# Kernel optimization log

Measured on AMD Instinct MI355X. Metric: run time of the kernel, lower is better.

## Reference

```python
import jax, jax.numpy as jnp
import numpy as np

N = 100000   # nodes
E = 1600000  # edges
F = 128      # input node features
H = 128      # hidden channels
G = 512      # graphs in batch
EPS = 1e-5   # BatchNorm eps


def setup_inputs() -> dict:
    key = jax.random.key(0)
    ks = jax.random.split(key, 24)
    x = jax.random.normal(ks[0], (N, F), jnp.float32)
    edge_index = jax.random.randint(ks[1], (2, E), 0, N)
    batch = jnp.sort(jax.random.randint(ks[2], (N,), 0, G))

    def lin_w(k, i, o):
        return jax.random.normal(k, (i, o), jnp.float32) / np.sqrt(i)

    inp = {
        "x": x, "edge_index": edge_index, "batch": batch,
        "W1": lin_w(ks[3], F, H), "b1": jnp.zeros((H,), jnp.float32),
        "g1": jnp.ones((H,), jnp.float32), "be1": jnp.zeros((H,), jnp.float32),
        "m1": 0.1 * jax.random.normal(ks[4], (H,), jnp.float32),
        "v1": jax.random.uniform(ks[5], (H,), jnp.float32) + 0.5,
        "W2": lin_w(ks[6], H, H), "b2": jnp.zeros((H,), jnp.float32),
        "g2": jnp.ones((H,), jnp.float32), "be2": jnp.zeros((H,), jnp.float32),
        "m2": 0.1 * jax.random.normal(ks[7], (H,), jnp.float32),
        "v2": jax.random.uniform(ks[8], (H,), jnp.float32) + 0.5,
        "W3": lin_w(ks[9], H, H), "b3": jnp.zeros((H,), jnp.float32),
        "g3": jnp.ones((H,), jnp.float32), "be3": jnp.zeros((H,), jnp.float32),
        "m3": 0.1 * jax.random.normal(ks[10], (H,), jnp.float32),
        "v3": jax.random.uniform(ks[11], (H,), jnp.float32) + 0.5,
        "Wl": lin_w(ks[12], H, 1), "bl": jnp.zeros((1,), jnp.float32),
    }
    return inp


def _gcn_norm(edge_index):
    # add self-loops, then symmetric normalization deg^-1/2 A_hat deg^-1/2
    loops = jnp.arange(N)
    src = jnp.concatenate([edge_index[0], loops])
    dst = jnp.concatenate([edge_index[1], loops])
    deg = jax.ops.segment_sum(jnp.ones_like(src, jnp.float32), dst, num_segments=N)
    dinv = jax.lax.rsqrt(jnp.maximum(deg, 1.0))
    norm = dinv[src] * dinv[dst]  # [E+N]
    return src, dst, norm


def _gcn_conv(x, W, b, src, dst, norm):
    h = x @ W                                    # [N,H] dense GEMM first (PyG order)
    msg = h[src] * norm[:, None]                 # gather + scale, [E+N,H]
    agg = jax.ops.segment_sum(msg, dst, num_segments=N)  # scatter-add
    return agg + b


def _bn_relu(x, g, be, m, v):
    # inference BatchNorm1d (running stats) + ReLU
    return jax.nn.relu((x - m) * jax.lax.rsqrt(v + EPS) * g + be)


def reference(x, edge_index, batch,
              W1, b1, g1, be1, m1, v1,
              W2, b2, g2, be2, m2, v2,
              W3, b3, g3, be3, m3, v3,
              Wl, bl):
    src, dst, norm = _gcn_norm(edge_index)
    h = _bn_relu(_gcn_conv(x, W1, b1, src, dst, norm), g1, be1, m1, v1)
    h = _bn_relu(_gcn_conv(h, W2, b2, src, dst, norm), g2, be2, m2, v2)
    h = _bn_relu(_gcn_conv(h, W3, b3, src, dst, norm), g3, be3, m3, v3)
    # global mean pool over graphs
    sums = jax.ops.segment_sum(h, batch, num_segments=G)           # [G,H]
    cnt = jax.ops.segment_sum(jnp.ones((N,), jnp.float32), batch, num_segments=G)
    pooled = sums / jnp.maximum(cnt, 1.0)[:, None]
    # dropout is identity at inference; final linear
    return pooled @ Wl + bl  # [G,1]
```

## Files before the change

### kernel.cpp

```cpp
#include <hip/hip_runtime.h>
#include <hip/hip_bf16.h>

#define NN 100000
#define NE 1600000
#define HD 128
#define NG 512
#define BN_EPS 1e-5f

#define GEMM_BLOCKS 1563

#define BIN_SHIFT 8
#define NBIN 391
#define TILE 16384
#define NBLK_BIN 98

typedef __attribute__((ext_vector_type(8))) short short8;
typedef __attribute__((ext_vector_type(4))) float floatx4;

__device__ __forceinline__ ushort f2bf(float f) {
    union { float f; uint u; } v; v.f = f;
    uint r = (v.u + 0x7FFF + ((v.u >> 16) & 1)) >> 16;
    return (ushort)r;
}
__device__ __forceinline__ float bflo(uint u) { union { uint u; float f; } v; v.u = u << 16; return v.f; }
__device__ __forceinline__ float bfhi(uint u) { union { uint u; float f; } v; v.u = u & 0xFFFF0000u; return v.f; }

__global__ void k_prep_all(const float* __restrict__ W1, const float* __restrict__ W2,
                           const float* __restrict__ W3,
                           ushort* __restrict__ Wt1, ushort* __restrict__ Wt2,
                           ushort* __restrict__ Wt3,
                           const float* __restrict__ b1, const float* __restrict__ g1,
                           const float* __restrict__ be1, const float* __restrict__ m1,
                           const float* __restrict__ v1,
                           const float* __restrict__ b2, const float* __restrict__ g2,
                           const float* __restrict__ be2, const float* __restrict__ m2,
                           const float* __restrict__ v2,
                           const float* __restrict__ b3, const float* __restrict__ g3,
                           const float* __restrict__ be3, const float* __restrict__ m3,
                           const float* __restrict__ v3,
                           float* scale1, float* shift1, float* scale2, float* shift2,
                           float* scale3, float* shift3,
                           const int* __restrict__ bat, float* __restrict__ invcnt,
                           float* __restrict__ out2d) {
    int blk = blockIdx.x, tid = threadIdx.x;
    if (blk < 192) {
        int w = blk >> 6;
        int i = (blk & 63) * 256 + tid;
        const float* W = (w == 0) ? W1 : (w == 1) ? W2 : W3;
        ushort* Wt = (w == 0) ? Wt1 : (w == 1) ? Wt2 : Wt3;
        int k = i >> 7, n = i & 127;
        Wt[n * 128 + k] = f2bf(W[i]);
    } else if (blk < 195) {
        if (tid < 128) {
            int l = blk - 192;
            const float *b, *g, *be, *m, *v;
            float *sc, *sh;
            if (l == 0)      { b = b1; g = g1; be = be1; m = m1; v = v1; sc = scale1; sh = shift1; }
            else if (l == 1) { b = b2; g = g2; be = be2; m = m2; v = v2; sc = scale2; sh = shift2; }
            else             { b = b3; g = g3; be = be3; m = m3; v = v3; sc = scale3; sh = shift3; }
            float s = g[tid] * rsqrtf(v[tid] + BN_EPS);
            sc[tid] = s;
            sh[tid] = (b[tid] - m[tid]) * s + be[tid];
        }
    } else {
        int g = (blk - 195) * 256 + tid;
        if (g < NG) {
            int lo = 0, hi = NN;
            while (lo < hi) { int mid = (lo + hi) >> 1; if (bat[mid] < g) lo = mid + 1; else hi = mid; }
            int lo2 = lo, hi2 = NN;
            while (lo2 < hi2) { int mid = (lo2 + hi2) >> 1; if (bat[mid] < g + 1) lo2 = mid + 1; else hi2 = mid; }
            int cnt = lo2 - lo;
            invcnt[g] = 1.f / fmaxf((float)cnt, 1.f);
#pragma unroll
            for (int i = 0; i < 8; ++i) out2d[g * 8 + i] = 0.f;
        }
    }
}

__launch_bounds__(256)
__global__ void k_fused1(const float* __restrict__ x, const ushort* __restrict__ Wt,
                         ushort* __restrict__ hs,
                         const int* __restrict__ dst, int* __restrict__ L) {
    __shared__ int lh[NBIN];
    const int tid = threadIdx.x;
    if (blockIdx.x >= GEMM_BLOCKS) {
        int blk = blockIdx.x - GEMM_BLOCKS;
        for (int i = tid; i < NBIN; i += 256) lh[i] = 0;
        __syncthreads();
        long base = (long)blk * TILE;
#pragma unroll 4
        for (int i = 0; i < TILE / 256; ++i) {
            long e = base + i * 256 + tid;
            if (e < NE) atomicAdd(&lh[dst[e] >> BIN_SHIFT], 1);
        }
        __syncthreads();
        for (int i = tid; i < NBIN; i += 256) L[i * NBLK_BIN + blk] = lh[i];
        return;
    }
    const int wave = tid >> 6, lane = tid & 63;
    const int m = lane & 15, kg = lane >> 4;
    const long row0 = (long)blockIdx.x * 64 + wave * 16;

    long arow = row0 + m;
    long arc = arow < NN ? arow : (NN - 1);
    const float* xf = x + arc * 128;
    short8 a[4];
#pragma unroll
    for (int s = 0; s < 4; ++s) {
        float4 f0 = *(const float4*)(xf + s * 32 + kg * 8);
        float4 f1 = *(const float4*)(xf + s * 32 + kg * 8 + 4);
        short8 t;
        t[0] = (short)f2bf(f0.x); t[1] = (short)f2bf(f0.y);
        t[2] = (short)f2bf(f0.z); t[3] = (short)f2bf(f0.w);
        t[4] = (short)f2bf(f1.x); t[5] = (short)f2bf(f1.y);
        t[6] = (short)f2bf(f1.z); t[7] = (short)f2bf(f1.w);
        a[s] = t;
    }

    floatx4 acc[8];
#pragma unroll
    for (int ct = 0; ct < 8; ++ct) acc[ct] = (floatx4){0.f, 0.f, 0.f, 0.f};

#pragma unroll
    for (int s = 0; s < 4; ++s) {
#pragma unroll
        for (int ct = 0; ct < 8; ++ct) {
            short8 b = *(const short8*)(Wt + (ct * 16 + m) * 128 + s * 32 + kg * 8);
            acc[ct] = __builtin_amdgcn_mfma_f32_16x16x32_bf16(a[s], b, acc[ct], 0, 0, 0);
        }
    }

#pragma unroll
    for (int r = 0; r < 4; ++r) {
        long orow = row0 + kg * 4 + r;
        if (orow < NN) {
#pragma unroll
            for (int ct = 0; ct < 8; ++ct)
                hs[orow * 128 + ct * 16 + m] = f2bf(acc[ct][r]);
        }
    }
}

__global__ void k_binscan(int* __restrict__ L, int* __restrict__ bin_ebase,
                          int* __restrict__ rs) {
    __shared__ int s[512];
    int t = threadIdx.x;
    int tot = 0;
    if (t < NBIN) {
        int run = 0;
        for (int b = 0; b < NBLK_BIN; ++b) {
            int h = L[t * NBLK_BIN + b];
            L[t * NBLK_BIN + b] = run;
            run += h;
        }
        tot = run;
    }
    s[t] = tot;
    __syncthreads();
    for (int o = 1; o < 512; o <<= 1) {
        int x = (t >= o) ? s[t - o] : 0;
        __syncthreads();
        s[t] += x;
        __syncthreads();
    }
    int excl = s[t] - tot;
    if (t < NBIN) {
        bin_ebase[t] = excl;
        for (int b = 0; b < NBLK_BIN; ++b) L[t * NBLK_BIN + b] += excl;
    }
    if (t == 0) { bin_ebase[NBIN] = NE; rs[NN] = NE; }
}

__launch_bounds__(256)
__global__ void k_binscatter(const int* __restrict__ src, const int* __restrict__ dst,
                             const int* __restrict__ L, uint* __restrict__ bpack) {
    __shared__ int off[NBIN];
    int t = threadIdx.x, blk = blockIdx.x;
    for (int i = t; i < NBIN; i += 256) off[i] = L[i * NBLK_BIN + blk];
    __syncthreads();
    long base = (long)blk * TILE;
#pragma unroll 4
    for (int i = 0; i < TILE / 256; ++i) {
        long e = base + i * 256 + t;
        if (e < NE) {
            int d = dst[e];
            int p = atomicAdd(&off[d >> BIN_SHIFT], 1);
            bpack[p] = (uint)src[e] | ((uint)(d & 255) << 24);
        }
    }
}

__launch_bounds__(256)
__global__ void k_bincsr(const uint* __restrict__ bpack, const int* __restrict__ bin_ebase,
                         int* __restrict__ rs, float* __restrict__ dinv,
                         int* __restrict__ csr) {
    __shared__ int cnt[256];
    __shared__ int sc[256];
    __shared__ int run[256];
    int t = threadIdx.x, b = blockIdx.x;
    int e0 = bin_ebase[b], e1 = bin_ebase[b + 1];
    cnt[t] = 0;
    __syncthreads();
    for (int e = e0 + t; e < e1; e += 256) atomicAdd(&cnt[bpack[e] >> 24], 1);
    __syncthreads();
    int c = cnt[t];
    sc[t] = c;
    __syncthreads();
    for (int o = 1; o < 256; o <<= 1) {
        int x = (t >= o) ? sc[t - o] : 0;
        __syncthreads();
        sc[t] += x;
        __syncthreads();
    }
    int excl = sc[t] - c;
    int node = (b << BIN_SHIFT) + t;
    if (node < NN) {
        rs[node] = e0 + excl;
        dinv[node] = rsqrtf((float)(c + 1));
    }
    run[t] = e0 + excl;
    __syncthreads();
    for (int e = e0 + t; e < e1; e += 256) {
        uint u = bpack[e];
        int p = atomicAdd(&run[u >> 24], 1);
        csr[p] = (int)(u & 0xFFFFFFu);
    }
}

#define WT_STRIDE 136
__launch_bounds__(256)
__global__ void k_gemm_l23(const ushort* __restrict__ xb, const ushort* __restrict__ Wt,
                           const float* __restrict__ dinv, ushort* __restrict__ hs) {
    __shared__ ushort sWt[128 * WT_STRIDE];
    const int tid = threadIdx.x;
    for (int i = tid; i < 2048; i += 256) {
        int row = i >> 4, seg = i & 15;
        *(uint4*)&sWt[row * WT_STRIDE + seg * 8] = *(const uint4*)(Wt + row * 128 + seg * 8);
    }
    __syncthreads();

    const int wave = tid >> 6, lane = tid & 63;
    const int m = lane & 15, kg = lane >> 4;
    const long row0 = (long)blockIdx.x * 64 + wave * 16;

    long arow = row0 + m;
    long arc = arow < NN ? arow : (NN - 1);
    short8 a[4];
#pragma unroll
    for (int s = 0; s < 4; ++s)
        a[s] = *(const short8*)(xb + arc * 128 + s * 32 + kg * 8);

    floatx4 acc[8];
#pragma unroll
    for (int ct = 0; ct < 8; ++ct) acc[ct] = (floatx4){0.f, 0.f, 0.f, 0.f};

#pragma unroll
    for (int s = 0; s < 4; ++s) {
#pragma unroll
        for (int ct = 0; ct < 8; ++ct) {
            short8 b = *(const short8*)&sWt[(ct * 16 + m) * WT_STRIDE + s * 32 + kg * 8];
            acc[ct] = __builtin_amdgcn_mfma_f32_16x16x32_bf16(a[s], b, acc[ct], 0, 0, 0);
        }
    }

#pragma unroll
    for (int r = 0; r < 4; ++r) {
        long orow = row0 + kg * 4 + r;
        if (orow < NN) {
            float dd = dinv[orow];
#pragma unroll
            for (int ct = 0; ct < 8; ++ct)
                hs[orow * 128 + ct * 16 + m] = f2bf(acc[ct][r] * dd);
        }
    }
}

template <bool SCALE_SRC, bool POOL>
__launch_bounds__(256)
__global__ void k_gather_w(const ushort* __restrict__ hs, const int* __restrict__ rs,
                           const int* __restrict__ csr, const float* __restrict__ dinv,
                           const float* __restrict__ scale, const float* __restrict__ shift,
                           ushort* __restrict__ xout,
                           const int* __restrict__ bat, const float* __restrict__ invcnt,
                           const float* __restrict__ Wl, float* __restrict__ out2d) {
    const int tid = threadIdx.x;
    const int d = blockIdx.x * 4 + (tid >> 6);
    const int lane = tid & 63;
    const int sub = lane >> 4;
    const int c0 = (lane & 15) * 8;

    const int e0 = rs[d], e1 = rs[d + 1];
    const float dd = dinv[d];

    float a0 = 0.f, a1 = 0.f, a2 = 0.f, a3 = 0.f,
          a4 = 0.f, a5 = 0.f, a6 = 0.f, a7 = 0.f;

    if (sub == 0) {
        uint4 sv = *(const uint4*)(hs + (long)d * 128 + c0);
        float w = SCALE_SRC ? dd : 1.0f;
        a0 = w * bflo(sv.x); a1 = w * bfhi(sv.x);
        a2 = w * bflo(sv.y); a3 = w * bfhi(sv.y);
        a4 = w * bflo(sv.z); a5 = w * bfhi(sv.z);
        a6 = w * bflo(sv.w); a7 = w * bfhi(sv.w);
    }

    int j = e0 + sub;
    int s0 = 0, s1 = 0, s2 = 0, s3 = 0;
    bool have = (j + 12 < e1);
    if (have) { s0 = csr[j]; s1 = csr[j + 4]; s2 = csr[j + 8]; s3 = csr[j + 12]; }
    while (have) {
        int jn = j + 16;
        bool nxt = (jn + 12 < e1);
        int n0 = 0, n1 = 0, n2 = 0, n3 = 0;
        if (nxt) { n0 = csr[jn]; n1 = csr[jn + 4]; n2 = csr[jn + 8]; n3 = csr[jn + 12]; }
        float w0 = 1.f, w1 = 1.f, w2 = 1.f, w3 = 1.f;
        if (SCALE_SRC) { w0 = dinv[s0]; w1 = dinv[s1]; w2 = dinv[s2]; w3 = dinv[s3]; }
        uint4 v0 = *(const uint4*)(hs + (long)s0 * 128 + c0);
        uint4 v1 = *(const uint4*)(hs + (long)s1 * 128 + c0);
        uint4 v2 = *(const uint4*)(hs + (long)s2 * 128 + c0);
        uint4 v3 = *(const uint4*)(hs + (long)s3 * 128 + c0);
        a0 += w0 * bflo(v0.x) + w1 * bflo(v1.x) + w2 * bflo(v2.x) + w3 * bflo(v3.x);
        a1 += w0 * bfhi(v0.x) + w1 * bfhi(v1.x) + w2 * bfhi(v2.x) + w3 * bfhi(v3.x);
        a2 += w0 * bflo(v0.y) + w1 * bflo(v1.y) + w2 * bflo(v2.y) + w3 * bflo(v3.y);
        a3 += w0 * bfhi(v0.y) + w1 * bfhi(v1.y) + w2 * bfhi(v2.y) + w3 * bfhi(v3.y);
        a4 += w0 * bflo(v0.z) + w1 * bflo(v1.z) + w2 * bflo(v2.z) + w3 * bflo(v3.z);
        a5 += w0 * bfhi(v0.z) + w1 * bfhi(v1.z) + w2 * bfhi(v2.z) + w3 * bfhi(v3.z);
        a6 += w0 * bflo(v0.w) + w1 * bflo(v1.w) + w2 * bflo(v2.w) + w3 * bflo(v3.w);
        a7 += w0 * bfhi(v0.w) + w1 * bfhi(v1.w) + w2 * bfhi(v2.w) + w3 * bfhi(v3.w);
        j = jn; s0 = n0; s1 = n1; s2 = n2; s3 = n3; have = nxt;
    }
    if (j < e1) {
        bool b1 = (j + 4) < e1, b2 = (j + 8) < e1;
        int t0 = csr[j];
        int t1 = b1 ? csr[j + 4] : t0;
        int t2 = b2 ? csr[j + 8] : t0;
        float w0 = SCALE_SRC ? dinv[t0] : 1.f;
        float w1 = b1 ? (SCALE_SRC ? dinv[t1] : 1.f) : 0.f;
        float w2 = b2 ? (SCALE_SRC ? dinv[t2] : 1.f) : 0.f;
        uint4 v0 = *(const uint4*)(hs + (long)t0 * 128 + c0);
        uint4 v1 = *(const uint4*)(hs + (long)t1 * 128 + c0);
        uint4 v2 = *(const uint4*)(hs + (long)t2 * 128 + c0);
        a0 += w0 * bflo(v0.x) + w1 * bflo(v1.x) + w2 * bflo(v2.x);
        a1 += w0 * bfhi(v0.x) + w1 * bfhi(v1.x) + w2 * bfhi(v2.x);
        a2 += w0 * bflo(v0.y) + w1 * bflo(v1.y) + w2 * bflo(v2.y);
        a3 += w0 * bfhi(v0.y) + w1 * bfhi(v1.y) + w2 * bfhi(v2.y);
        a4 += w0 * bflo(v0.z) + w1 * bflo(v1.z) + w2 * bflo(v2.z);
        a5 += w0 * bfhi(v0.z) + w1 * bfhi(v1.z) + w2 * bfhi(v2.z);
        a6 += w0 * bflo(v0.w) + w1 * bflo(v1.w) + w2 * bflo(v2.w);
        a7 += w0 * bfhi(v0.w) + w1 * bfhi(v1.w) + w2 * bfhi(v2.w);
    }

    a0 += __shfl_xor(a0, 16); a1 += __shfl_xor(a1, 16);
    a2 += __shfl_xor(a2, 16); a3 += __shfl_xor(a3, 16);
    a4 += __shfl_xor(a4, 16); a5 += __shfl_xor(a5, 16);
    a6 += __shfl_xor(a6, 16); a7 += __shfl_xor(a7, 16);
    a0 += __shfl_xor(a0, 32); a1 += __shfl_xor(a1, 32);
    a2 += __shfl_xor(a2, 32); a3 += __shfl_xor(a3, 32);
    a4 += __shfl_xor(a4, 32); a5 += __shfl_xor(a5, 32);
    a6 += __shfl_xor(a6, 32); a7 += __shfl_xor(a7, 32);

    float pd = 0.f;
    if (sub == 0) {
        float4 sca = *(const float4*)(scale + c0);
        float4 scb = *(const float4*)(scale + c0 + 4);
        float4 sha = *(const float4*)(shift + c0);
        float4 shb = *(const float4*)(shift + c0 + 4);
        float r0 = fmaxf(dd * a0 * sca.x + sha.x, 0.f);
        float r1 = fmaxf(dd * a1 * sca.y + sha.y, 0.f);
        float r2 = fmaxf(dd * a2 * sca.z + sha.z, 0.f);
        float r3 = fmaxf(dd * a3 * sca.w + sha.w, 0.f);
        float r4 = fmaxf(dd * a4 * scb.x + shb.x, 0.f);
        float r5 = fmaxf(dd * a5 * scb.y + shb.y, 0.f);
        float r6 = fmaxf(dd * a6 * scb.z + shb.z, 0.f);
        float r7 = fmaxf(dd * a7 * scb.w + shb.w, 0.f);
        if constexpr (POOL) {
            float4 wa = *(const float4*)(Wl + c0);
            float4 wb = *(const float4*)(Wl + c0 + 4);
            pd = r0 * wa.x + r1 * wa.y + r2 * wa.z + r3 * wa.w +
                 r4 * wb.x + r5 * wb.y + r6 * wb.z + r7 * wb.w;
        } else {
            uint4 o;
            o.x = (uint)f2bf(r0) | ((uint)f2bf(r1) << 16);
            o.y = (uint)f2bf(r2) | ((uint)f2bf(r3) << 16);
            o.z = (uint)f2bf(r4) | ((uint)f2bf(r5) << 16);
            o.w = (uint)f2bf(r6) | ((uint)f2bf(r7) << 16);
            *(uint4*)(xout + (long)d * 128 + c0) = o;
        }
    }
    if constexpr (POOL) {
        pd += __shfl_xor(pd, 1);
        pd += __shfl_xor(pd, 2);
        pd += __shfl_xor(pd, 4);
        pd += __shfl_xor(pd, 8);
        if (lane == 0) {
            int g = bat[d];
            atomicAdd(&out2d[g * 8 + (d & 7)], pd * invcnt[g]);
        }
    }
}

__global__ void k_final(const float* __restrict__ out2d, const float* __restrict__ bl,
                        float* __restrict__ out) {
    int g = blockIdx.x * 256 + threadIdx.x;
    if (g >= NG) return;
    float s = bl[0];
#pragma unroll
    for (int i = 0; i < 8; ++i) s += out2d[g * 8 + i];
    out[g] = s;
}

extern "C" void kernel_launch(void* const* d_in, const int* in_sizes, int n_in,
                              void* d_out, int out_size, void* d_ws, size_t ws_size,
                              hipStream_t stream) {
    const float* x   = (const float*)d_in[0];
    const int*   ei  = (const int*)d_in[1];
    const int*   bat = (const int*)d_in[2];
    const float* W1  = (const float*)d_in[3];
    const float* b1  = (const float*)d_in[4];
    const float* g1  = (const float*)d_in[5];
    const float* be1 = (const float*)d_in[6];
    const float* m1  = (const float*)d_in[7];
    const float* v1  = (const float*)d_in[8];
    const float* W2  = (const float*)d_in[9];
    const float* b2  = (const float*)d_in[10];
    const float* g2  = (const float*)d_in[11];
    const float* be2 = (const float*)d_in[12];
    const float* m2  = (const float*)d_in[13];
    const float* v2  = (const float*)d_in[14];
    const float* W3  = (const float*)d_in[15];
    const float* b3  = (const float*)d_in[16];
    const float* g3  = (const float*)d_in[17];
    const float* be3 = (const float*)d_in[18];
    const float* m3  = (const float*)d_in[19];
    const float* v3  = (const float*)d_in[20];
    const float* Wl  = (const float*)d_in[21];
    const float* bl  = (const float*)d_in[22];
    float* out = (float*)d_out;

    const int* srcp = ei;
    const int* dstp = ei + NE;

    char* ws = (char*)d_ws;
    size_t off = 0;
    auto alloc = [&](size_t bytes) { char* p = ws + off; off += (bytes + 255) & ~255ULL; return p; };
    float*  dinv     = (float*) alloc(NN * 4);
    int*    rs       = (int*)   alloc((NN + 1) * 4);
    int*    L        = (int*)   alloc((size_t)NBIN * NBLK_BIN * 4);
    int*    bin_ebase= (int*)   alloc((NBIN + 1) * 4);
    uint*   bpack    = (uint*)  alloc((size_t)NE * 4);
    int*    csr      = (int*)   alloc((size_t)NE * 4);
    float*  scale1 = (float*) alloc(HD * 4);
    float*  shift1 = (float*) alloc(HD * 4);
    float*  scale2 = (float*) alloc(HD * 4);
    float*  shift2 = (float*) alloc(HD * 4);
    float*  scale3 = (float*) alloc(HD * 4);
    float*  shift3 = (float*) alloc(HD * 4);
    float*  invcnt = (float*) alloc(NG * 4);
    float*  out2d  = (float*) alloc(NG * 8 * 4);
    ushort* Wt1    = (ushort*)alloc(128 * 128 * 2);
    ushort* Wt2    = (ushort*)alloc(128 * 128 * 2);
    ushort* Wt3    = (ushort*)alloc(128 * 128 * 2);
    ushort* hs     = (ushort*)alloc((size_t)NN * HD * 2);
    ushort* xbuf   = (ushort*)alloc((size_t)NN * HD * 2);

    const int gath_grid = NN / 4;

    k_prep_all<<<197, 256, 0, stream>>>(W1, W2, W3, Wt1, Wt2, Wt3,
                                        b1, g1, be1, m1, v1, b2, g2, be2, m2, v2,
                                        b3, g3, be3, m3, v3,
                                        scale1, shift1, scale2, shift2, scale3, shift3,
                                        bat, invcnt, out2d);

    k_fused1<<<GEMM_BLOCKS + NBLK_BIN, 256, 0, stream>>>(x, Wt1, hs, dstp, L);

    k_binscan<<<1, 512, 0, stream>>>(L, bin_ebase, rs);
    k_binscatter<<<NBLK_BIN, 256, 0, stream>>>(srcp, dstp, L, bpack);
    k_bincsr<<<NBIN, 256, 0, stream>>>(bpack, bin_ebase, rs, dinv, csr);

    k_gather_w<true, false><<<gath_grid, 256, 0, stream>>>(
        hs, rs, csr, dinv, scale1, shift1, xbuf, nullptr, nullptr, nullptr, nullptr);
    k_gemm_l23<<<GEMM_BLOCKS, 256, 0, stream>>>(xbuf, Wt2, dinv, hs);
    k_gather_w<false, false><<<gath_grid, 256, 0, stream>>>(
        hs, rs, csr, dinv, scale2, shift2, xbuf, nullptr, nullptr, nullptr, nullptr);
    k_gemm_l23<<<GEMM_BLOCKS, 256, 0, stream>>>(xbuf, Wt3, dinv, hs);
    k_gather_w<false, true><<<gath_grid, 256, 0, stream>>>(
        hs, rs, csr, dinv, scale3, shift3, nullptr, bat, invcnt, Wl, out2d);

    k_final<<<2, 256, 0, stream>>>(out2d, bl, out);
}
```

Baseline: 513.5 us.

## Parallelize bin scan across blocks, shrink binning tiles, use persistent gather grid

The edge-binning count/scatter now uses 391 smaller tiles instead of 98 large ones, giving more parallel blocks. The single-block serial bin scan is replaced by a two-stage scan: one block per bin scans per-tile counts, and a second kernel scans the bin totals. The bin base offset is then added inside the scatter. The three gather kernels switch from one wave per node to a fixed 2048-block grid-stride loop, which cuts block launch overhead but may worsen load balance across nodes of uneven degree.

```diff
diff --git a/kernel.cpp b/kernel.cpp
--- a/kernel.cpp
+++ b/kernel.cpp
@@ -8,11 +8,12 @@
 #define BN_EPS 1e-5f
 
 #define GEMM_BLOCKS 1563
+#define GATH_BLOCKS 2048
 
 #define BIN_SHIFT 8
 #define NBIN 391
-#define TILE 16384
-#define NBLK_BIN 98
+#define TILE 4096
+#define NBLK_BIN 391
 
 typedef __attribute__((ext_vector_type(8))) short short8;
 typedef __attribute__((ext_vector_type(4))) float floatx4;
@@ -141,21 +142,28 @@
     }
 }
 
-__global__ void k_binscan(int* __restrict__ L, int* __restrict__ bin_ebase,
-                          int* __restrict__ rs) {
+__global__ void k_scanA(int* __restrict__ L, int* __restrict__ binTot) {
+    __shared__ int s[512];
+    int b = blockIdx.x, t = threadIdx.x;
+    int v = (t < NBLK_BIN) ? L[b * NBLK_BIN + t] : 0;
+    s[t] = v;
+    __syncthreads();
+    for (int o = 1; o < 512; o <<= 1) {
+        int x = (t >= o) ? s[t - o] : 0;
+        __syncthreads();
+        s[t] += x;
+        __syncthreads();
+    }
+    if (t < NBLK_BIN) L[b * NBLK_BIN + t] = s[t] - v;
+    if (t == 511) binTot[b] = s[511];
+}
+
+__global__ void k_scanB(const int* __restrict__ binTot, int* __restrict__ bin_ebase,
+                        int* __restrict__ rs) {
     __shared__ int s[512];
     int t = threadIdx.x;
-    int tot = 0;
-    if (t < NBIN) {
-        int run = 0;
-        for (int b = 0; b < NBLK_BIN; ++b) {
-            int h = L[t * NBLK_BIN + b];
-            L[t * NBLK_BIN + b] = run;
-            run += h;
-        }
-        tot = run;
-    }
-    s[t] = tot;
+    int v = (t < NBIN) ? binTot[t] : 0;
+    s[t] = v;
     __syncthreads();
     for (int o = 1; o < 512; o <<= 1) {
         int x = (t >= o) ? s[t - o] : 0;
@@ -163,20 +171,17 @@
         s[t] += x;
         __syncthreads();
     }
-    int excl = s[t] - tot;
-    if (t < NBIN) {
-        bin_ebase[t] = excl;
-        for (int b = 0; b < NBLK_BIN; ++b) L[t * NBLK_BIN + b] += excl;
-    }
+    if (t < NBIN) bin_ebase[t] = s[t] - v;
     if (t == 0) { bin_ebase[NBIN] = NE; rs[NN] = NE; }
 }
 
 __launch_bounds__(256)
 __global__ void k_binscatter(const int* __restrict__ src, const int* __restrict__ dst,
-                             const int* __restrict__ L, uint* __restrict__ bpack) {
+                             const int* __restrict__ L, const int* __restrict__ bin_ebase,
+                             uint* __restrict__ bpack) {
     __shared__ int off[NBIN];
     int t = threadIdx.x, blk = blockIdx.x;
-    for (int i = t; i < NBIN; i += 256) off[i] = L[i * NBLK_BIN + blk];
+    for (int i = t; i < NBIN; i += 256) off[i] = L[i * NBLK_BIN + blk] + bin_ebase[i];
     __syncthreads();
     long base = (long)blk * TILE;
 #pragma unroll 4
@@ -284,117 +289,120 @@
                            const int* __restrict__ bat, const float* __restrict__ invcnt,
                            const float* __restrict__ Wl, float* __restrict__ out2d) {
     const int tid = threadIdx.x;
-    const int d = blockIdx.x * 4 + (tid >> 6);
+    const int gw = blockIdx.x * 4 + (tid >> 6);
+    const int NW = GATH_BLOCKS * 4;
     const int lane = tid & 63;
     const int sub = lane >> 4;
     const int c0 = (lane & 15) * 8;
 
-    const int e0 = rs[d], e1 = rs[d + 1];
-    const float dd = dinv[d];
-
-    float a0 = 0.f, a1 = 0.f, a2 = 0.f, a3 = 0.f,
-          a4 = 0.f, a5 = 0.f, a6 = 0.f, a7 = 0.f;
-
-    if (sub == 0) {
-        uint4 sv = *(const uint4*)(hs + (long)d * 128 + c0);
-        float w = SCALE_SRC ? dd : 1.0f;
-        a0 = w * bflo(sv.x); a1 = w * bfhi(sv.x);
-        a2 = w * bflo(sv.y); a3 = w * bfhi(sv.y);
-        a4 = w * bflo(sv.z); a5 = w * bfhi(sv.z);
-        a6 = w * bflo(sv.w); a7 = w * bfhi(sv.w);
-    }
-
-    int j = e0 + sub;
-    int s0 = 0, s1 = 0, s2 = 0, s3 = 0;
-    bool have = (j + 12 < e1);
-    if (have) { s0 = csr[j]; s1 = csr[j + 4]; s2 = csr[j + 8]; s3 = csr[j + 12]; }
-    while (have) {
-        int jn = j + 16;
-        bool nxt = (jn + 12 < e1);
-        int n0 = 0, n1 = 0, n2 = 0, n3 = 0;
-        if (nxt) { n0 = csr[jn]; n1 = csr[jn + 4]; n2 = csr[jn + 8]; n3 = csr[jn + 12]; }
-        float w0 = 1.f, w1 = 1.f, w2 = 1.f, w3 = 1.f;
-        if (SCALE_SRC) { w0 = dinv[s0]; w1 = dinv[s1]; w2 = dinv[s2]; w3 = dinv[s3]; }
-        uint4 v0 = *(const uint4*)(hs + (long)s0 * 128 + c0);
-        uint4 v1 = *(const uint4*)(hs + (long)s1 * 128 + c0);
-        uint4 v2 = *(const uint4*)(hs + (long)s2 * 128 + c0);
-        uint4 v3 = *(const uint4*)(hs + (long)s3 * 128 + c0);
-        a0 += w0 * bflo(v0.x) + w1 * bflo(v1.x) + w2 * bflo(v2.x) + w3 * bflo(v3.x);
-        a1 += w0 * bfhi(v0.x) + w1 * bfhi(v1.x) + w2 * bfhi(v2.x) + w3 * bfhi(v3.x);
-        a2 += w0 * bflo(v0.y) + w1 * bflo(v1.y) + w2 * bflo(v2.y) + w3 * bflo(v3.y);
-        a3 += w0 * bfhi(v0.y) + w1 * bfhi(v1.y) + w2 * bfhi(v2.y) + w3 * bfhi(v3.y);
-        a4 += w0 * bflo(v0.z) + w1 * bflo(v1.z) + w2 * bflo(v2.z) + w3 * bflo(v3.z);
-        a5 += w0 * bfhi(v0.z) + w1 * bfhi(v1.z) + w2 * bfhi(v2.z) + w3 * bfhi(v3.z);
-        a6 += w0 * bflo(v0.w) + w1 * bflo(v1.w) + w2 * bflo(v2.w) + w3 * bflo(v3.w);
-        a7 += w0 * bfhi(v0.w) + w1 * bfhi(v1.w) + w2 * bfhi(v2.w) + w3 * bfhi(v3.w);
-        j = jn; s0 = n0; s1 = n1; s2 = n2; s3 = n3; have = nxt;
-    }
-    if (j < e1) {
-        bool b1 = (j + 4) < e1, b2 = (j + 8) < e1;
-        int t0 = csr[j];
-        int t1 = b1 ? csr[j + 4] : t0;
-        int t2 = b2 ? csr[j + 8] : t0;
-        float w0 = SCALE_SRC ? dinv[t0] : 1.f;
-        float w1 = b1 ? (SCALE_SRC ? dinv[t1] : 1.f) : 0.f;
-        float w2 = b2 ? (SCALE_SRC ? dinv[t2] : 1.f) : 0.f;
-        uint4 v0 = *(const uint4*)(hs + (long)t0 * 128 + c0);
-        uint4 v1 = *(const uint4*)(hs + (long)t1 * 128 + c0);
-        uint4 v2 = *(const uint4*)(hs + (long)t2 * 128 + c0);
-        a0 += w0 * bflo(v0.x) + w1 * bflo(v1.x) + w2 * bflo(v2.x);
-        a1 += w0 * bfhi(v0.x) + w1 * bfhi(v1.x) + w2 * bfhi(v2.x);
-        a2 += w0 * bflo(v0.y) + w1 * bflo(v1.y) + w2 * bflo(v2.y);
-        a3 += w0 * bfhi(v0.y) + w1 * bfhi(v1.y) + w2 * bfhi(v2.y);
-        a4 += w0 * bflo(v0.z) + w1 * bflo(v1.z) + w2 * bflo(v2.z);
-        a5 += w0 * bfhi(v0.z) + w1 * bfhi(v1.z) + w2 * bfhi(v2.z);
-        a6 += w0 * bflo(v0.w) + w1 * bflo(v1.w) + w2 * bflo(v2.w);
-        a7 += w0 * bfhi(v0.w) + w1 * bfhi(v1.w) + w2 * bfhi(v2.w);
-    }
-
-    a0 += __shfl_xor(a0, 16); a1 += __shfl_xor(a1, 16);
-    a2 += __shfl_xor(a2, 16); a3 += __shfl_xor(a3, 16);
-    a4 += __shfl_xor(a4, 16); a5 += __shfl_xor(a5, 16);
-    a6 += __shfl_xor(a6, 16); a7 += __shfl_xor(a7, 16);
-    a0 += __shfl_xor(a0, 32); a1 += __shfl_xor(a1, 32);
-    a2 += __shfl_xor(a2, 32); a3 += __shfl_xor(a3, 32);
-    a4 += __shfl_xor(a4, 32); a5 += __shfl_xor(a5, 32);
-    a6 += __shfl_xor(a6, 32); a7 += __shfl_xor(a7, 32);
-
-    float pd = 0.f;
-    if (sub == 0) {
-        float4 sca = *(const float4*)(scale + c0);
-        float4 scb = *(const float4*)(scale + c0 + 4);
-        float4 sha = *(const float4*)(shift + c0);
-        float4 shb = *(const float4*)(shift + c0 + 4);
-        float r0 = fmaxf(dd * a0 * sca.x + sha.x, 0.f);
-        float r1 = fmaxf(dd * a1 * sca.y + sha.y, 0.f);
-        float r2 = fmaxf(dd * a2 * sca.z + sha.z, 0.f);
-        float r3 = fmaxf(dd * a3 * sca.w + sha.w, 0.f);
-        float r4 = fmaxf(dd * a4 * scb.x + shb.x, 0.f);
-        float r5 = fmaxf(dd * a5 * scb.y + shb.y, 0.f);
-        float r6 = fmaxf(dd * a6 * scb.z + shb.z, 0.f);
-        float r7 = fmaxf(dd * a7 * scb.w + shb.w, 0.f);
+    for (int d = gw; d < NN; d += NW) {
+        const int e0 = rs[d], e1 = rs[d + 1];
+        const float dd = dinv[d];
+
+        float a0 = 0.f, a1 = 0.f, a2 = 0.f, a3 = 0.f,
+              a4 = 0.f, a5 = 0.f, a6 = 0.f, a7 = 0.f;
+
+        if (sub == 0) {
+            uint4 sv = *(const uint4*)(hs + (long)d * 128 + c0);
+            float w = SCALE_SRC ? dd : 1.0f;
+            a0 = w * bflo(sv.x); a1 = w * bfhi(sv.x);
+            a2 = w * bflo(sv.y); a3 = w * bfhi(sv.y);
+            a4 = w * bflo(sv.z); a5 = w * bfhi(sv.z);
+            a6 = w * bflo(sv.w); a7 = w * bfhi(sv.w);
+        }
+
+        int j = e0 + sub;
+        int s0 = 0, s1 = 0, s2 = 0, s3 = 0;
+        bool have = (j + 12 < e1);
+        if (have) { s0 = csr[j]; s1 = csr[j + 4]; s2 = csr[j + 8]; s3 = csr[j + 12]; }
+        while (have) {
+            int jn = j + 16;
+            bool nxt = (jn + 12 < e1);
+            int n0 = 0, n1 = 0, n2 = 0, n3 = 0;
+            if (nxt) { n0 = csr[jn]; n1 = csr[jn + 4]; n2 = csr[jn + 8]; n3 = csr[jn + 12]; }
+            float w0 = 1.f, w1 = 1.f, w2 = 1.f, w3 = 1.f;
+            if (SCALE_SRC) { w0 = dinv[s0]; w1 = dinv[s1]; w2 = dinv[s2]; w3 = dinv[s3]; }
+            uint4 v0 = *(const uint4*)(hs + (long)s0 * 128 + c0);
+            uint4 v1 = *(const uint4*)(hs + (long)s1 * 128 + c0);
+            uint4 v2 = *(const uint4*)(hs + (long)s2 * 128 + c0);
+            uint4 v3 = *(const uint4*)(hs + (long)s3 * 128 + c0);
+            a0 += w0 * bflo(v0.x) + w1 * bflo(v1.x) + w2 * bflo(v2.x) + w3 * bflo(v3.x);
+            a1 += w0 * bfhi(v0.x) + w1 * bfhi(v1.x) + w2 * bfhi(v2.x) + w3 * bfhi(v3.x);
+            a2 += w0 * bflo(v0.y) + w1 * bflo(v1.y) + w2 * bflo(v2.y) + w3 * bflo(v3.y);
+            a3 += w0 * bfhi(v0.y) + w1 * bfhi(v1.y) + w2 * bfhi(v2.y) + w3 * bfhi(v3.y);
+            a4 += w0 * bflo(v0.z) + w1 * bflo(v1.z) + w2 * bflo(v2.z) + w3 * bflo(v3.z);
+            a5 += w0 * bfhi(v0.z) + w1 * bfhi(v1.z) + w2 * bfhi(v2.z) + w3 * bfhi(v3.z);
+            a6 += w0 * bflo(v0.w) + w1 * bflo(v1.w) + w2 * bflo(v2.w) + w3 * bflo(v3.w);
+            a7 += w0 * bfhi(v0.w) + w1 * bfhi(v1.w) + w2 * bfhi(v2.w) + w3 * bfhi(v3.w);
+            j = jn; s0 = n0; s1 = n1; s2 = n2; s3 = n3; have = nxt;
+        }
+        if (j < e1) {
+            bool b1 = (j + 4) < e1, b2 = (j + 8) < e1;
+            int t0 = csr[j];
+            int t1 = b1 ? csr[j + 4] : t0;
+            int t2 = b2 ? csr[j + 8] : t0;
+            float w0 = SCALE_SRC ? dinv[t0] : 1.f;
+            float w1 = b1 ? (SCALE_SRC ? dinv[t1] : 1.f) : 0.f;
+            float w2 = b2 ? (SCALE_SRC ? dinv[t2] : 1.f) : 0.f;
+            uint4 v0 = *(const uint4*)(hs + (long)t0 * 128 + c0);
+            uint4 v1 = *(const uint4*)(hs + (long)t1 * 128 + c0);
+            uint4 v2 = *(const uint4*)(hs + (long)t2 * 128 + c0);
+            a0 += w0 * bflo(v0.x) + w1 * bflo(v1.x) + w2 * bflo(v2.x);
+            a1 += w0 * bfhi(v0.x) + w1 * bfhi(v1.x) + w2 * bfhi(v2.x);
+            a2 += w0 * bflo(v0.y) + w1 * bflo(v1.y) + w2 * bflo(v2.y);
+            a3 += w0 * bfhi(v0.y) + w1 * bfhi(v1.y) + w2 * bfhi(v2.y);
+            a4 += w0 * bflo(v0.z) + w1 * bflo(v1.z) + w2 * bflo(v2.z);
+            a5 += w0 * bfhi(v0.z) + w1 * bfhi(v1.z) + w2 * bfhi(v2.z);
+            a6 += w0 * bflo(v0.w) + w1 * bflo(v1.w) + w2 * bflo(v2.w);
+            a7 += w0 * bfhi(v0.w) + w1 * bfhi(v1.w) + w2 * bfhi(v2.w);
+        }
+
+        a0 += __shfl_xor(a0, 16); a1 += __shfl_xor(a1, 16);
+        a2 += __shfl_xor(a2, 16); a3 += __shfl_xor(a3, 16);
+        a4 += __shfl_xor(a4, 16); a5 += __shfl_xor(a5, 16);
+        a6 += __shfl_xor(a6, 16); a7 += __shfl_xor(a7, 16);
+        a0 += __shfl_xor(a0, 32); a1 += __shfl_xor(a1, 32);
+        a2 += __shfl_xor(a2, 32); a3 += __shfl_xor(a3, 32);
+        a4 += __shfl_xor(a4, 32); a5 += __shfl_xor(a5, 32);
+        a6 += __shfl_xor(a6, 32); a7 += __shfl_xor(a7, 32);
+
+        float pd = 0.f;
+        if (sub == 0) {
+            float4 sca = *(const float4*)(scale + c0);
+            float4 scb = *(const float4*)(scale + c0 + 4);
+            float4 sha = *(const float4*)(shift + c0);
+            float4 shb = *(const float4*)(shift + c0 + 4);
+            float r0 = fmaxf(dd * a0 * sca.x + sha.x, 0.f);
+            float r1 = fmaxf(dd * a1 * sca.y + sha.y, 0.f);
+            float r2 = fmaxf(dd * a2 * sca.z + sha.z, 0.f);
+            float r3 = fmaxf(dd * a3 * sca.w + sha.w, 0.f);
+            float r4 = fmaxf(dd * a4 * scb.x + shb.x, 0.f);
+            float r5 = fmaxf(dd * a5 * scb.y + shb.y, 0.f);
+            float r6 = fmaxf(dd * a6 * scb.z + shb.z, 0.f);
+            float r7 = fmaxf(dd * a7 * scb.w + shb.w, 0.f);
+            if constexpr (POOL) {
+                float4 wa = *(const float4*)(Wl + c0);
+                float4 wb = *(const float4*)(Wl + c0 + 4);
+                pd = r0 * wa.x + r1 * wa.y + r2 * wa.z + r3 * wa.w +
+                     r4 * wb.x + r5 * wb.y + r6 * wb.z + r7 * wb.w;
+            } else {
+                uint4 o;
+                o.x = (uint)f2bf(r0) | ((uint)f2bf(r1) << 16);
+                o.y = (uint)f2bf(r2) | ((uint)f2bf(r3) << 16);
+                o.z = (uint)f2bf(r4) | ((uint)f2bf(r5) << 16);
+                o.w = (uint)f2bf(r6) | ((uint)f2bf(r7) << 16);
+                *(uint4*)(xout + (long)d * 128 + c0) = o;
+            }
+        }
         if constexpr (POOL) {
-            float4 wa = *(const float4*)(Wl + c0);
-            float4 wb = *(const float4*)(Wl + c0 + 4);
-            pd = r0 * wa.x + r1 * wa.y + r2 * wa.z + r3 * wa.w +
-                 r4 * wb.x + r5 * wb.y + r6 * wb.z + r7 * wb.w;
-        } else {
-            uint4 o;
-            o.x = (uint)f2bf(r0) | ((uint)f2bf(r1) << 16);
-            o.y = (uint)f2bf(r2) | ((uint)f2bf(r3) << 16);
-            o.z = (uint)f2bf(r4) | ((uint)f2bf(r5) << 16);
-            o.w = (uint)f2bf(r6) | ((uint)f2bf(r7) << 16);
-            *(uint4*)(xout + (long)d * 128 + c0) = o;
-        }
-    }
-    if constexpr (POOL) {
-        pd += __shfl_xor(pd, 1);
-        pd += __shfl_xor(pd, 2);
-        pd += __shfl_xor(pd, 4);
-        pd += __shfl_xor(pd, 8);
-        if (lane == 0) {
-            int g = bat[d];
-            atomicAdd(&out2d[g * 8 + (d & 7)], pd * invcnt[g]);
+            pd += __shfl_xor(pd, 1);
+            pd += __shfl_xor(pd, 2);
+            pd += __shfl_xor(pd, 4);
+            pd += __shfl_xor(pd, 8);
+            if (lane == 0) {
+                int g = bat[d];
+                atomicAdd(&out2d[g * 8 + (d & 7)], pd * invcnt[g]);
+            }
         }
     }
 }
@@ -446,6 +454,7 @@
     float*  dinv     = (float*) alloc(NN * 4);
     int*    rs       = (int*)   alloc((NN + 1) * 4);
     int*    L        = (int*)   alloc((size_t)NBIN * NBLK_BIN * 4);
+    int*    binTot   = (int*)   alloc((NBIN + 1) * 4);
     int*    bin_ebase= (int*)   alloc((NBIN + 1) * 4);
     uint*   bpack    = (uint*)  alloc((size_t)NE * 4);
     int*    csr      = (int*)   alloc((size_t)NE * 4);
@@ -463,8 +472,6 @@
     ushort* hs     = (ushort*)alloc((size_t)NN * HD * 2);
     ushort* xbuf   = (ushort*)alloc((size_t)NN * HD * 2);
 
-    const int gath_grid = NN / 4;
-
     k_prep_all<<<197, 256, 0, stream>>>(W1, W2, W3, Wt1, Wt2, Wt3,
                                         b1, g1, be1, m1, v1, b2, g2, be2, m2, v2,
                                         b3, g3, be3, m3, v3,
@@ -473,17 +480,18 @@
 
     k_fused1<<<GEMM_BLOCKS + NBLK_BIN, 256, 0, stream>>>(x, Wt1, hs, dstp, L);
 
-    k_binscan<<<1, 512, 0, stream>>>(L, bin_ebase, rs);
-    k_binscatter<<<NBLK_BIN, 256, 0, stream>>>(srcp, dstp, L, bpack);
+    k_scanA<<<NBIN, 512, 0, stream>>>(L, binTot);
+    k_scanB<<<1, 512, 0, stream>>>(binTot, bin_ebase, rs);
+    k_binscatter<<<NBLK_BIN, 256, 0, stream>>>(srcp, dstp, L, bin_ebase, bpack);
     k_bincsr<<<NBIN, 256, 0, stream>>>(bpack, bin_ebase, rs, dinv, csr);
 
-    k_gather_w<true, false><<<gath_grid, 256, 0, stream>>>(
+    k_gather_w<true, false><<<GATH_BLOCKS, 256, 0, stream>>>(
         hs, rs, csr, dinv, scale1, shift1, xbuf, nullptr, nullptr, nullptr, nullptr);
     k_gemm_l23<<<GEMM_BLOCKS, 256, 0, stream>>>(xbuf, Wt2, dinv, hs);
-    k_gather_w<false, false><<<gath_grid, 256, 0, stream>>>(
+    k_gather_w<false, false><<<GATH_BLOCKS, 256, 0, stream>>>(
         hs, rs, csr, dinv, scale2, shift2, xbuf, nullptr, nullptr, nullptr, nullptr);
     k_gemm_l23<<<GEMM_BLOCKS, 256, 0, stream>>>(xbuf, Wt3, dinv, hs);
-    k_gather_w<false, true><<<gath_grid, 256, 0, stream>>>(
+    k_gather_w<false, true><<<GATH_BLOCKS, 256, 0, stream>>>(
         hs, rs, csr, dinv, scale3, shift3, nullptr, bat, invcnt, Wl, out2d);
 
     k_final<<<2, 256, 0, stream>>>(out2d, bl, out);
```

New measurement: 515.6 us. Within noise of the previous version (+0.4%).
